# Performance work log

Hardware: AMD Instinct MI355X
Metric: run time of the kernel (lower is better)

## Reference

```python
import jax, jax.numpy as jnp
import numpy as np

HIDDEN, INPUT_DIM, OUTPUT_DIM, SEQ_LEN, BATCH = 1024, 1, 10, 784, 512


def make_discrete_hippo(N, L):
    # HiPPO-LegS matrix: A[n,k] = -sqrt(2n+1)sqrt(2k+1) for n>k, -(n+1) on diag; B[n]=sqrt(2n+1)
    q = np.arange(N, dtype=np.float64)
    P = np.sqrt(1.0 + 2.0 * q)
    A = -(np.tril(np.outer(P, P)) - np.diag(q))
    B = P[:, None]  # (N, 1)
    # bilinear (Tustin) discretization with step = 1/L
    step = 1.0 / L
    I = np.eye(N)
    M = np.linalg.inv(I - (step / 2.0) * A)
    Ad = M @ (I + (step / 2.0) * A)
    Bd = step * (M @ B)
    return jnp.asarray(Ad, jnp.float32), jnp.asarray(Bd, jnp.float32)


def setup_inputs() -> dict:
    key = jax.random.key(0)
    k1, k2, k3 = jax.random.split(key, 3)
    x = jax.random.normal(k1, (BATCH, SEQ_LEN, 1), jnp.float32)
    # C: xavier_uniform-like scale, shape (input_dim, hidden_dim)
    C = jax.random.normal(k2, (INPUT_DIM, HIDDEN), jnp.float32) / np.sqrt(HIDDEN).astype(np.float32)
    # final Dense(output_dim): kernel (input_dim, output_dim), bias (output_dim,)
    W = jax.random.normal(k3, (INPUT_DIM, OUTPUT_DIM), jnp.float32)
    b = jnp.zeros((OUTPUT_DIM,), jnp.float32)
    return {"x": x, "C": C, "W": W, "b": b}


def reference(x, C, W, b):
    Ad, Bd = make_discrete_hippo(HIDDEN, SEQ_LEN)  # constants (not learned)
    AdT = Ad.T                       # (N, N)
    Bvec = Bd[:, 0]                  # (N,)
    us = jnp.moveaxis(x[..., 0], 1, 0)  # (seq, batch) -- scan over time axis
    h0 = jnp.zeros((x.shape[0], HIDDEN), x.dtype)

    def step(h, u):
        # h_next = tanh(A h^T + B u)^T  ==  tanh(h @ A^T + u[:,None]*B)
        h_next = jnp.tanh(h @ AdT + u[:, None] * Bvec[None, :])  # (batch, N)
        y = h_next @ C.T                                         # (batch, input_dim)
        return h_next, y

    _, ys = jax.lax.scan(step, h0, us)  # ys: (seq, batch, input_dim)
    # Dense applied to all timesteps then [:, -1, :] == Dense on last timestep
    return ys[-1] @ W + b  # (batch, output_dim)
```

## Files before the change

kernel.cpp:

```cpp
#include <hip/hip_runtime.h>
#include <math.h>


#define SEQ     784
#define OUT_DIM 10
#define NW      8
#define CH      16
#define NCH     (SEQ/CH)
#define EPL     4

typedef float v2f __attribute__((ext_vector_type(2)));

#if __has_builtin(__builtin_elementwise_fma)
__device__ __forceinline__ v2f fma2(v2f a, v2f b, v2f c) {
    return __builtin_elementwise_fma(a, b, c);
}
#else
__device__ __forceinline__ v2f fma2(v2f a, v2f b, v2f c) {
    v2f r; r.x = fmaf(a.x, b.x, c.x); r.y = fmaf(a.y, b.y, c.y); return r;
}
#endif

#if __has_builtin(__builtin_amdgcn_exp2f)
#define EXP2F(x) __builtin_amdgcn_exp2f(x)
#else
#define EXP2F(x) __expf(0.69314718055994531f * (x))
#endif

template<int CTRL, int ROW_MASK>
__device__ __forceinline__ float dpp_mov(float src, float old) {
    return __int_as_float(__builtin_amdgcn_update_dpp(
        __float_as_int(old), __float_as_int(src), CTRL, ROW_MASK, 0xf, false));
}

__global__ __launch_bounds__(512, 2)
void ssm_hippo_scan(const float* __restrict__ x,
                    const float* __restrict__ C,
                    const float* __restrict__ W,
                    const float* __restrict__ bvec,
                    float* __restrict__ out)
{
    const int b0   = blockIdx.x * 2;
    const int tid  = threadIdx.x;
    const int wv   = tid >> 6;
    const int lane = tid & 63;
    const int lh   = lane & 31;
    const int h    = lane >> 5;

    __shared__ __align__(16) float u_s[2][SEQ];
    __shared__ __align__(16) float tot_s[NW-1][2][SEQ];
    __shared__ double part_s[NW][2];

    for (int t = tid; t < SEQ; t += 512) {
        u_s[0][t] = x[(b0 + 0) * SEQ + t];
        u_s[1][t] = x[(b0 + 1) * SEQ + t];
    }

    const double hdt  = 0.5 / (double)SEQ;
    const double L2E2 = 2.0 * 1.4426950408889634;

    v2f upc01, upc23, ivd01, ivd23, cB01, cB23;
    v2f ka01, ka23, c20_30, c21_31;
    float t10, t32;
    float Alev0, Alev1, Alev2, Alev3, Alev4, Aexcl;
    float PhiW, c2, n2c2;
    {
        double p[EPL], d[EPL], a[EPL], pdin[EPL], hp[EPL];
#pragma unroll
        for (int i = 0; i < EPL; ++i) {
            const int n = wv * 128 + lh * EPL + i;
            p[i]    = sqrt(1.0 + 2.0 * (double)n);
            d[i]    = 1.0 + hdt * (double)(n + 1);
            a[i]    = 1.0 - hdt * p[i] * p[i] / d[i];
            pdin[i] = p[i] / d[i];
            hp[i]   = 2.0 * hdt * p[i] / d[i];
        }
        upc01 = (v2f){(float)(L2E2 * hdt * p[0]), (float)(L2E2 * hdt * p[1])};
        upc23 = (v2f){(float)(L2E2 * hdt * p[2]), (float)(L2E2 * hdt * p[3])};
        ivd01 = (v2f){(float)(2.0 / d[0]), (float)(2.0 / d[1])};
        ivd23 = (v2f){(float)(2.0 / d[2]), (float)(2.0 / d[3])};
        ka01  = (v2f){(float)(-hp[0]), (float)(-hp[1] * a[0])};
        ka23  = (v2f){(float)(-hp[2] * a[0]*a[1]),
                      (float)(-hp[3] * a[0]*a[1]*a[2])};
        cB01  = (v2f){(float)(a[1]*a[2]*a[3] * pdin[0]),
                      (float)(a[2]*a[3] * pdin[1])};
        cB23  = (v2f){(float)(a[3] * pdin[2]), (float)(pdin[3])};
        t10   = (float)(-hp[1] * pdin[0]);
        c20_30= (v2f){(float)(-hp[2] * a[1] * pdin[0]),
                      (float)(-hp[3] * a[2] * a[1] * pdin[0])};
        c21_31= (v2f){(float)(-hp[2] * pdin[1]),
                      (float)(-hp[3] * a[2] * pdin[1])};
        t32   = (float)(-hp[3] * pdin[2]);

        float A = (float)(a[0]*a[1]*a[2]*a[3]);
        Alev0 = A; A *= dpp_mov<0x111, 0xf>(A, 1.0f);
        Alev1 = A; A *= dpp_mov<0x112, 0xf>(A, 1.0f);
        Alev2 = A; A *= dpp_mov<0x114, 0xf>(A, 1.0f);
        Alev3 = A; A *= dpp_mov<0x118, 0xf>(A, 1.0f);
        Alev4 = A; A *= dpp_mov<0x142, 0xa>(A, 1.0f);
        const float Ae_raw = dpp_mov<0x111, 0xf>(A, 1.0f);
        const float Ae_fix = dpp_mov<0x142, 0xa>(A, 1.0f);
        Aexcl = (lh == 16) ? Ae_fix : Ae_raw;

        double np = 1.0, dp = 1.0;
        for (int n = wv * 128; n < wv * 128 + 128; ++n) {
            np *= 1.0 - hdt * (double)n;
            dp *= 1.0 + hdt * (double)(n + 1);
        }
        PhiW = (float)(np / dp);

        c2   = (float)L2E2;
        n2c2 = (float)(-2.0 * L2E2);
    }

    const bool fixlane = (lh == 16);
    const v2f  c2v = (v2f){c2, c2};

    __syncthreads();

    v2f m01 = (v2f){0.0f, 0.0f}, m23 = (v2f){0.0f, 0.0f};
    float Bf = 0.0f;

#pragma unroll 1
    for (int tick = 0; tick < NCH + NW - 1; ++tick) {
        const int ch = tick - wv;
        if (0 <= ch && ch < NCH) {
            float4 u4[CH/4];
            float  Tin[CH];
            {
                const float4* up = (const float4*)&u_s[h][ch * CH];
#pragma unroll
                for (int q = 0; q < CH/4; ++q) u4[q] = up[q];
            }
            if (wv == 0) {
#pragma unroll
                for (int k = 0; k < CH; ++k) Tin[k] = 0.0f;
            } else {
                const float4* bp = (const float4*)&tot_s[wv - 1][h][ch * CH];
#pragma unroll
                for (int q = 0; q < CH/4; ++q) {
                    const float4 v0 = bp[q];
                    Tin[4*q+0] = v0.x; Tin[4*q+1] = v0.y;
                    Tin[4*q+2] = v0.z; Tin[4*q+3] = v0.w;
                }
            }
            float Bacc[CH];

#pragma unroll
            for (int k = 0; k < CH; ++k) {
                const float u = ((const float*)&u4[k>>2])[k&3];
                const v2f  uu = (v2f){u, u};

                const v2f w01 = fma2(upc01, uu, m01);
                const v2f w23 = fma2(upc23, uu, m23);

                const v2f bb01 = fma2(ivd01, w01, -m01);
                const v2f bb23 = fma2(ivd23, w23, -m23);

                const float pre = fmaf(t32, w23.x, bb23.y);
                const float g1t = fmaf(t10, w01.x, bb01.y);
                const v2f w0s = (v2f){w01.x, w01.x};
                const v2f w1s = (v2f){w01.y, w01.y};

                const v2f bt = fma2(cB23, w23, cB01 * w01);
                float B = bt.x + bt.y;

                float Tr;
                asm volatile(
                    "s_nop 1\n\t"
                    "v_fmac_f32_dpp %0, %0, %1 row_shr:1 row_mask:0xf bank_mask:0xf bound_ctrl:0"
                    : "+v"(B) : "v"(Alev0));
                v2f tri23 = fma2(c21_31, w1s, (v2f){bb23.x, pre});
                asm volatile(
                    "s_nop 1\n\t"
                    "v_fmac_f32_dpp %0, %0, %1 row_shr:2 row_mask:0xf bank_mask:0xf bound_ctrl:0"
                    : "+v"(B) : "v"(Alev1));
                tri23 = fma2(c20_30, w0s, tri23);
                asm volatile(
                    "s_nop 1\n\t"
                    "v_fmac_f32_dpp %0, %0, %1 row_shr:4 row_mask:0xf bank_mask:0xf bound_ctrl:0"
                    : "+v"(B) : "v"(Alev2));
                const v2f gb01 = (v2f){bb01.x, g1t};
                asm volatile(
                    "s_nop 1\n\t"
                    "v_fmac_f32_dpp %0, %0, %1 row_shr:8 row_mask:0xf bank_mask:0xf bound_ctrl:0"
                    : "+v"(B) : "v"(Alev3));
                asm volatile(
                    "s_nop 1\n\t"
                    "v_fmac_f32_dpp %0, %0, %1 row_bcast:15 row_mask:0xa bank_mask:0xf"
                    : "+v"(B) : "v"(Alev4));
                asm volatile(
                    "s_nop 1\n\t"
                    "v_mov_b32_dpp %0, %1 row_shr:1 row_mask:0xf bank_mask:0xf bound_ctrl:0"
                    : "=v"(Tr) : "v"(B));
                asm volatile(
                    "s_nop 1\n\t"
                    "v_mov_b32_dpp %0, %1 row_bcast:15 row_mask:0xa bank_mask:0xf"
                    : "+v"(Bf) : "v"(B));
                Bacc[k] = B;

                const float Tst  = fixlane ? Bf : Tr;
                const float Tent = fmaf(Aexcl, Tin[k], Tst);
                const v2f  TentV = (v2f){Tent, Tent};

                const v2f g01 = fma2(ka01, TentV, gb01);
                const v2f g23 = fma2(ka23, TentV, tri23);

                const float e0 = EXP2F(fminf(g01.x, 30.0f));
                const float e1 = EXP2F(fminf(g01.y, 30.0f));
                const float e2 = EXP2F(fminf(g23.x, 30.0f));
                const float e3 = EXP2F(fminf(g23.y, 30.0f));
                const v2f q01 = (v2f){e0, e1} + 1.0f;
                const v2f q23 = (v2f){e2, e3} + 1.0f;
                const float p01 = q01.x * q01.y, p23 = q23.x * q23.y;
                const float ip  = __builtin_amdgcn_rcpf(p01 * p23);
                const float tt  = n2c2 * ip;
                const float s01 = tt * p23;
                const float s23 = tt * p01;
                const v2f q01s = __builtin_shufflevector(q01, q01, 1, 0);
                const v2f q23s = __builtin_shufflevector(q23, q23, 1, 0);
                m01 = fma2((v2f){s01, s01}, q01s, c2v);
                m23 = fma2((v2f){s23, s23}, q23s, c2v);
            }

            if (wv < NW - 1 && lh == 31) {
                float4* tp = (float4*)&tot_s[wv][h][ch * CH];
#pragma unroll
                for (int q = 0; q < CH/4; ++q)
                    tp[q] = make_float4(
                        fmaf(PhiW, Tin[4*q+0], Bacc[4*q+0]),
                        fmaf(PhiW, Tin[4*q+1], Bacc[4*q+1]),
                        fmaf(PhiW, Tin[4*q+2], Bacc[4*q+2]),
                        fmaf(PhiW, Tin[4*q+3], Bacc[4*q+3]));
            }
        }
        __syncthreads();
    }

    double acc = 0.0;
    {
        const int base = wv * 128 + lh * EPL;
        acc = fma((double)C[base + 0], (double)m01.x, acc);
        acc = fma((double)C[base + 1], (double)m01.y, acc);
        acc = fma((double)C[base + 2], (double)m23.x, acc);
        acc = fma((double)C[base + 3], (double)m23.y, acc);
    }
#pragma unroll
    for (int off = 16; off > 0; off >>= 1)
        acc += __shfl_down(acc, off, 32);
    if (lh == 0) part_s[wv][h] = acc;
    __syncthreads();
    if (tid < 2 * OUT_DIM) {
        const int q = tid / OUT_DIM, j = tid - q * OUT_DIM;
        double tot = 0.0;
#pragma unroll
        for (int wq = 0; wq < NW; ++wq) tot += part_s[wq][q];
        tot *= 0.34657359027997264;
        out[(b0 + q) * OUT_DIM + j] =
            (float)fma(tot, (double)W[j], (double)bvec[j]);
    }
}

extern "C" void kernel_launch(void* const* d_in, const int* in_sizes, int n_in,
                              void* d_out, int out_size, void* d_ws, size_t ws_size,
                              hipStream_t stream) {
    const float* x  = (const float*)d_in[0];
    const float* C  = (const float*)d_in[1];
    const float* W  = (const float*)d_in[2];
    const float* bv = (const float*)d_in[3];
    float* out      = (float*)d_out;
    hipLaunchKernelGGL(ssm_hippo_scan, dim3(256), dim3(512), 0, stream,
                       x, C, W, bv, out);
}
```

Baseline: 239.3 us.

## Replace exp-based tanh with clamped rational approximation and compiler DPP scan

Swaps the exp2+reciprocal tanh evaluation for a clamped Padé-style rational polynomial (degree 7/6) sharing one reciprocal across four lanes, removing transcendental unit usage from the serial recurrence. It also replaces hand-written inline-asm DPP prefix-scan steps with update_dpp builtins and a single row_bcast-based exclusive shift, letting the compiler schedule them. The scaling constants change accordingly (no log2e folding, no final rescale). The rational approximation with clamp at 4.8 trades accuracy for fewer special-function ops and may drift over 784 steps.

```diff
diff --git a/kernel.cpp b/kernel.cpp
--- a/kernel.cpp
+++ b/kernel.cpp
@@ -21,16 +21,15 @@
 }
 #endif
 
-#if __has_builtin(__builtin_amdgcn_exp2f)
-#define EXP2F(x) __builtin_amdgcn_exp2f(x)
-#else
-#define EXP2F(x) __expf(0.69314718055994531f * (x))
-#endif
-
 template<int CTRL, int ROW_MASK>
 __device__ __forceinline__ float dpp_mov(float src, float old) {
     return __int_as_float(__builtin_amdgcn_update_dpp(
         __float_as_int(old), __float_as_int(src), CTRL, ROW_MASK, 0xf, false));
+}
+template<int CTRL>
+__device__ __forceinline__ float dpp_bc0(float src) {
+    return __int_as_float(__builtin_amdgcn_update_dpp(
+        0, __float_as_int(src), CTRL, 0xf, 0xf, true));
 }
 
 __global__ __launch_bounds__(512, 2)
@@ -56,14 +55,13 @@
         u_s[1][t] = x[(b0 + 1) * SEQ + t];
     }
 
-    const double hdt  = 0.5 / (double)SEQ;
-    const double L2E2 = 2.0 * 1.4426950408889634;
+    const double hdt = 0.5 / (double)SEQ;
 
     v2f upc01, upc23, ivd01, ivd23, cB01, cB23;
     v2f ka01, ka23, c20_30, c21_31;
     float t10, t32;
     float Alev0, Alev1, Alev2, Alev3, Alev4, Aexcl;
-    float PhiW, c2, n2c2;
+    float PhiW;
     {
         double p[EPL], d[EPL], a[EPL], pdin[EPL], hp[EPL];
 #pragma unroll
@@ -75,8 +73,8 @@
             pdin[i] = p[i] / d[i];
             hp[i]   = 2.0 * hdt * p[i] / d[i];
         }
-        upc01 = (v2f){(float)(L2E2 * hdt * p[0]), (float)(L2E2 * hdt * p[1])};
-        upc23 = (v2f){(float)(L2E2 * hdt * p[2]), (float)(L2E2 * hdt * p[3])};
+        upc01 = (v2f){(float)(hdt * p[0]), (float)(hdt * p[1])};
+        upc23 = (v2f){(float)(hdt * p[2]), (float)(hdt * p[3])};
         ivd01 = (v2f){(float)(2.0 / d[0]), (float)(2.0 / d[1])};
         ivd23 = (v2f){(float)(2.0 / d[2]), (float)(2.0 / d[3])};
         ka01  = (v2f){(float)(-hp[0]), (float)(-hp[1] * a[0])};
@@ -108,18 +106,20 @@
             dp *= 1.0 + hdt * (double)(n + 1);
         }
         PhiW = (float)(np / dp);
-
-        c2   = (float)L2E2;
-        n2c2 = (float)(-2.0 * L2E2);
-    }
-
-    const bool fixlane = (lh == 16);
-    const v2f  c2v = (v2f){c2, c2};
+    }
+
+    const bool not32 = (lane != 32);
+    const v2f CN2 = (v2f){  378.0f,   378.0f};
+    const v2f CN1 = (v2f){17325.0f, 17325.0f};
+    const v2f CC0 = (v2f){135135.0f, 135135.0f};
+    const v2f CD3 = (v2f){   28.0f,    28.0f};
+    const v2f CD2 = (v2f){ 3150.0f,  3150.0f};
+    const v2f CD1 = (v2f){62370.0f, 62370.0f};
+    const float YC = 4.8f;
 
     __syncthreads();
 
     v2f m01 = (v2f){0.0f, 0.0f}, m23 = (v2f){0.0f, 0.0f};
-    float Bf = 0.0f;
 
 #pragma unroll 1
     for (int tick = 0; tick < NCH + NW - 1; ++tick) {
@@ -157,70 +157,55 @@
                 const v2f bb01 = fma2(ivd01, w01, -m01);
                 const v2f bb23 = fma2(ivd23, w23, -m23);
 
-                const float pre = fmaf(t32, w23.x, bb23.y);
                 const float g1t = fmaf(t10, w01.x, bb01.y);
                 const v2f w0s = (v2f){w01.x, w01.x};
                 const v2f w1s = (v2f){w01.y, w01.y};
+                v2f tri23 = fma2(c21_31, w1s,
+                                 (v2f){bb23.x, fmaf(t32, w23.x, bb23.y)});
+                tri23 = fma2(c20_30, w0s, tri23);
 
                 const v2f bt = fma2(cB23, w23, cB01 * w01);
                 float B = bt.x + bt.y;
 
-                float Tr;
-                asm volatile(
-                    "s_nop 1\n\t"
-                    "v_fmac_f32_dpp %0, %0, %1 row_shr:1 row_mask:0xf bank_mask:0xf bound_ctrl:0"
-                    : "+v"(B) : "v"(Alev0));
-                v2f tri23 = fma2(c21_31, w1s, (v2f){bb23.x, pre});
-                asm volatile(
-                    "s_nop 1\n\t"
-                    "v_fmac_f32_dpp %0, %0, %1 row_shr:2 row_mask:0xf bank_mask:0xf bound_ctrl:0"
-                    : "+v"(B) : "v"(Alev1));
-                tri23 = fma2(c20_30, w0s, tri23);
-                asm volatile(
-                    "s_nop 1\n\t"
-                    "v_fmac_f32_dpp %0, %0, %1 row_shr:4 row_mask:0xf bank_mask:0xf bound_ctrl:0"
-                    : "+v"(B) : "v"(Alev2));
+                B = fmaf(Alev0, dpp_bc0<0x111>(B), B);
+                B = fmaf(Alev1, dpp_bc0<0x112>(B), B);
+                B = fmaf(Alev2, dpp_bc0<0x114>(B), B);
+                B = fmaf(Alev3, dpp_bc0<0x118>(B), B);
+                B = fmaf(Alev4, dpp_mov<0x142, 0xa>(B, 0.0f), B);
+                Bacc[k] = B;
+
+                const float Tst_raw = dpp_bc0<0x138>(B);
+                const float Tst     = not32 ? Tst_raw : 0.0f;
+                const float Tent    = fmaf(Aexcl, Tin[k], Tst);
+                const v2f  TentV    = (v2f){Tent, Tent};
+
                 const v2f gb01 = (v2f){bb01.x, g1t};
-                asm volatile(
-                    "s_nop 1\n\t"
-                    "v_fmac_f32_dpp %0, %0, %1 row_shr:8 row_mask:0xf bank_mask:0xf bound_ctrl:0"
-                    : "+v"(B) : "v"(Alev3));
-                asm volatile(
-                    "s_nop 1\n\t"
-                    "v_fmac_f32_dpp %0, %0, %1 row_bcast:15 row_mask:0xa bank_mask:0xf"
-                    : "+v"(B) : "v"(Alev4));
-                asm volatile(
-                    "s_nop 1\n\t"
-                    "v_mov_b32_dpp %0, %1 row_shr:1 row_mask:0xf bank_mask:0xf bound_ctrl:0"
-                    : "=v"(Tr) : "v"(B));
-                asm volatile(
-                    "s_nop 1\n\t"
-                    "v_mov_b32_dpp %0, %1 row_bcast:15 row_mask:0xa bank_mask:0xf"
-                    : "+v"(Bf) : "v"(B));
-                Bacc[k] = B;
-
-                const float Tst  = fixlane ? Bf : Tr;
-                const float Tent = fmaf(Aexcl, Tin[k], Tst);
-                const v2f  TentV = (v2f){Tent, Tent};
-
-                const v2f g01 = fma2(ka01, TentV, gb01);
-                const v2f g23 = fma2(ka23, TentV, tri23);
-
-                const float e0 = EXP2F(fminf(g01.x, 30.0f));
-                const float e1 = EXP2F(fminf(g01.y, 30.0f));
-                const float e2 = EXP2F(fminf(g23.x, 30.0f));
-                const float e3 = EXP2F(fminf(g23.y, 30.0f));
-                const v2f q01 = (v2f){e0, e1} + 1.0f;
-                const v2f q23 = (v2f){e2, e3} + 1.0f;
-                const float p01 = q01.x * q01.y, p23 = q23.x * q23.y;
+                const v2f y01  = fma2(ka01, TentV, gb01);
+                const v2f y23  = fma2(ka23, TentV, tri23);
+
+                v2f x01, x23;
+                x01.x = __builtin_amdgcn_fmed3f(y01.x, -YC, YC);
+                x01.y = __builtin_amdgcn_fmed3f(y01.y, -YC, YC);
+                x23.x = __builtin_amdgcn_fmed3f(y23.x, -YC, YC);
+                x23.y = __builtin_amdgcn_fmed3f(y23.y, -YC, YC);
+                const v2f t01 = x01 * x01, t23 = x23 * x23;
+                const v2f n01 = fma2(fma2(t01 + CN2, t01, CN1), t01, CC0);
+                const v2f n23 = fma2(fma2(t23 + CN2, t23, CN1), t23, CC0);
+                const v2f num01 = x01 * n01;
+                const v2f num23 = x23 * n23;
+                const v2f d01 = fma2(fma2(fma2(CD3, t01, CD2), t01, CD1),
+                                     t01, CC0);
+                const v2f d23 = fma2(fma2(fma2(CD3, t23, CD2), t23, CD1),
+                                     t23, CC0);
+                const float p01 = d01.x * d01.y;
+                const float p23 = d23.x * d23.y;
                 const float ip  = __builtin_amdgcn_rcpf(p01 * p23);
-                const float tt  = n2c2 * ip;
-                const float s01 = tt * p23;
-                const float s23 = tt * p01;
-                const v2f q01s = __builtin_shufflevector(q01, q01, 1, 0);
-                const v2f q23s = __builtin_shufflevector(q23, q23, 1, 0);
-                m01 = fma2((v2f){s01, s01}, q01s, c2v);
-                m23 = fma2((v2f){s23, s23}, q23s, c2v);
+                const float i01 = p23 * ip;
+                const float i23 = p01 * ip;
+                const v2f nd01 = num01 * __builtin_shufflevector(d01, d01, 1, 0);
+                const v2f nd23 = num23 * __builtin_shufflevector(d23, d23, 1, 0);
+                m01 = nd01 * (v2f){i01, i01};
+                m23 = nd23 * (v2f){i23, i23};
             }
 
             if (wv < NW - 1 && lh == 31) {
@@ -255,7 +240,6 @@
         double tot = 0.0;
 #pragma unroll
         for (int wq = 0; wq < NW; ++wq) tot += part_s[wq][q];
-        tot *= 0.34657359027997264;
         out[(b0 + q) * OUT_DIM + j] =
             (float)fma(tot, (double)W[j], (double)bvec[j]);
     }
```

Result: slower. 270.5 us (+13.0%).
